# Kernel tuning notes

Measured on AMD Instinct MI355X. Metric: run time of the kernel, lower is better.

Reference implementation:

```python
import jax, jax.numpy as jnp
import numpy as np

N = 100000   # nodes
E = 1600000  # directed edges
F_IN = 100
H = 256
N_LABELS = 19
BN_EPS = 1e-5


def setup_inputs() -> dict:
    key = jax.random.key(0)
    ks = jax.random.split(key, 12)
    p = lambda k, shape, s=0.05: jax.random.normal(k, shape, dtype=jnp.float32) * s
    return {
        "x": jax.random.normal(ks[0], (N, F_IN), dtype=jnp.float32),
        "edge_index": jax.random.randint(ks[1], (2, E), 0, N, dtype=jnp.int32),
        "W1": p(ks[2], (F_IN, F_IN)), "b1": jnp.zeros((F_IN,), jnp.float32),
        "W2": p(ks[3], (F_IN, F_IN)), "b2": jnp.zeros((F_IN,), jnp.float32),
        "W3": p(ks[4], (F_IN, H)),   "b3": jnp.zeros((H,), jnp.float32),
        "fc1_W": p(ks[5], (H, H)),   "fc1_b": jnp.zeros((H,), jnp.float32),
        "fc2a_W": p(ks[6], (H, 128)), "fc2a_b": jnp.zeros((128,), jnp.float32),
        "bn_gamma": jnp.ones((128,), jnp.float32), "bn_beta": jnp.zeros((128,), jnp.float32),
        "fc2b_W": p(ks[7], (128, N_LABELS)), "fc2b_b": jnp.zeros((N_LABELS,), jnp.float32),
    }


def _gcn_conv(x, W, b, src, dst, dinv):
    """PyG GCNConv with add_self_loops + symmetric normalization.
    out[dst] += dinv[src]*dinv[dst] * (x @ W)[src], plus self-loop term, plus bias.
    """
    n = x.shape[0]
    xw = x @ W  # [N, out]
    norm = dinv[src] * dinv[dst]  # [E]
    agg = jax.ops.segment_sum(xw[src] * norm[:, None], dst, num_segments=n)
    agg = agg + xw * (dinv * dinv)[:, None]  # self loops (i -> i)
    return agg + b


def reference(x, edge_index, W1, b1, W2, b2, W3, b3, fc1_W, fc1_b,
              fc2a_W, fc2a_b, bn_gamma, bn_beta, fc2b_W, fc2b_b):
    src, dst = edge_index[0], edge_index[1]
    n = x.shape[0]
    # degree of augmented graph (A + I), computed on targets (sum aggregation)
    deg = jax.ops.segment_sum(jnp.ones((src.shape[0],), x.dtype), dst, num_segments=n) + 1.0
    dinv = jax.lax.rsqrt(deg)

    h = jnp.clip(x, -0.4, 0.4)
    h = jax.nn.relu(_gcn_conv(h, W1, b1, src, dst, dinv))
    h = jax.nn.relu(_gcn_conv(h, W2, b2, src, dst, dinv))
    h = jax.nn.relu(_gcn_conv(h, W3, b3, src, dst, dinv))
    h = jax.nn.relu(h @ fc1_W + fc1_b)
    # fc2: Linear -> BatchNorm1d (train mode, batch stats) -> ReLU -> Linear
    h = h @ fc2a_W + fc2a_b
    mu = jnp.mean(h, axis=0)
    var = jnp.mean(jnp.square(h - mu), axis=0)  # biased var, as torch BN uses
    h = (h - mu) * jax.lax.rsqrt(var + BN_EPS) * bn_gamma + bn_beta
    h = jax.nn.relu(h)
    logits = h @ fc2b_W + fc2b_b
    return jax.nn.log_softmax(logits, axis=1)
```

## Files before the change

### kernel.cpp

```cpp
#include <hip/hip_runtime.h>
#include <hip/hip_bf16.h>

#define N_NODES 100000
#define N_EDGES 1600000
#define F_IN_DIM 100
#define F_IN_PAD 104
#define H_DIM 256
#define BN_DIM 128
#define N_LABELS 19
#define BN_EPS 1e-5f

#define BUCKET_SHIFT 8
#define NB 391
#define EPB 4096
#define PB 391

typedef __attribute__((ext_vector_type(8))) short bf16x8;
typedef __attribute__((ext_vector_type(4))) short s16x4;
typedef __attribute__((ext_vector_type(4))) float f32x4;

static __device__ inline short f2bf(float f) {
    __hip_bfloat16 h = __float2bfloat16(f);
    return *(short*)&h;
}
static __device__ inline float bf2f(short s) {
    unsigned u = ((unsigned)(unsigned short)s) << 16;
    return __builtin_bit_cast(float, u);
}

__global__ __launch_bounds__(256) void part_hist_kernel(const int* __restrict__ dst,
                                                        int* __restrict__ part_hist, int E)
{
    __shared__ int h[NB];
    int tid = threadIdx.x;
    for (int i = tid; i < NB; i += 256) h[i] = 0;
    __syncthreads();
    int base = blockIdx.x * EPB;
    int end = min(base + EPB, E);
    for (int e = base + tid; e < end; e += 256)
        atomicAdd(&h[dst[e] >> BUCKET_SHIFT], 1);
    __syncthreads();
    for (int i = tid; i < NB; i += 256) part_hist[blockIdx.x * NB + i] = h[i];
}

__global__ __launch_bounds__(512) void bucket_total_kernel(const int* __restrict__ part_hist,
                                                           int* __restrict__ bucket_total)
{
    __shared__ int ls[512];
    int b = blockIdx.x;
    int s = 0;
    for (int p = threadIdx.x; p < PB; p += 512) s += part_hist[p * NB + b];
    ls[threadIdx.x] = s;
    __syncthreads();
    for (int off = 256; off > 0; off >>= 1) {
        if (threadIdx.x < off) ls[threadIdx.x] += ls[threadIdx.x + off];
        __syncthreads();
    }
    if (threadIdx.x == 0) bucket_total[b] = ls[0];
}

__global__ __launch_bounds__(512) void bucket_scan_kernel(const int* __restrict__ bucket_total,
                                                          int* __restrict__ bucket_base)
{
    __shared__ int ls[512];
    int tid = threadIdx.x;
    ls[tid] = (tid < NB) ? bucket_total[tid] : 0;
    __syncthreads();
    for (int off = 1; off < 512; off <<= 1) {
        int v = ls[tid];
        int add = (tid >= off) ? ls[tid - off] : 0;
        __syncthreads();
        ls[tid] = v + add;
        __syncthreads();
    }
    if (tid < NB) bucket_base[tid] = (tid > 0) ? ls[tid - 1] : 0;
    if (tid == 0) bucket_base[NB] = ls[NB - 1];
}

__global__ __launch_bounds__(512) void part_offset_kernel(int* __restrict__ part_hist,
                                                          const int* __restrict__ bucket_base)
{
    __shared__ int ls[512];
    int b = blockIdx.x;
    int tid = threadIdx.x;
    int v = (tid < PB) ? part_hist[tid * NB + b] : 0;
    ls[tid] = v;
    __syncthreads();
    for (int off = 1; off < 512; off <<= 1) {
        int x = ls[tid];
        int add = (tid >= off) ? ls[tid - off] : 0;
        __syncthreads();
        ls[tid] = x + add;
        __syncthreads();
    }
    if (tid < PB) part_hist[tid * NB + b] = bucket_base[b] + ((tid > 0) ? ls[tid - 1] : 0);
}

__global__ __launch_bounds__(256) void partition_kernel(const int* __restrict__ src,
                                                        const int* __restrict__ dst,
                                                        const int* __restrict__ part_hist,
                                                        int* __restrict__ ep, int E)
{
    __shared__ int cur[NB];
    int tid = threadIdx.x;
    for (int i = tid; i < NB; i += 256) cur[i] = part_hist[blockIdx.x * NB + i];
    __syncthreads();
    int base = blockIdx.x * EPB;
    int end = min(base + EPB, E);
    for (int e = base + tid; e < end; e += 256) {
        int d = dst[e];
        int s = src[e];
        int pos = atomicAdd(&cur[d >> BUCKET_SHIFT], 1);
        ep[pos] = (s << 8) | (d & 255);
    }
}

__global__ __launch_bounds__(256) void bucket_csr_kernel(const int* __restrict__ ep,
                                                         const int* __restrict__ bucket_base,
                                                         int* __restrict__ row_start,
                                                         float* __restrict__ dinv,
                                                         int* __restrict__ src_sorted, int N, int E)
{
    __shared__ int h[256], sc[256], cur[256];
    int b = blockIdx.x;
    int tid = threadIdx.x;
    int e0 = bucket_base[b], e1 = bucket_base[b + 1];
    int node0 = b << BUCKET_SHIFT;
    int nn = min(256, N - node0);

    h[tid] = 0;
    __syncthreads();
    for (int e = e0 + tid; e < e1; e += 256)
        atomicAdd(&h[ep[e] & 255], 1);
    __syncthreads();

    sc[tid] = h[tid];
    __syncthreads();
    for (int off = 1; off < 256; off <<= 1) {
        int v = sc[tid];
        int add = (tid >= off) ? sc[tid - off] : 0;
        __syncthreads();
        sc[tid] = v + add;
        __syncthreads();
    }
    int excl = e0 + ((tid > 0) ? sc[tid - 1] : 0);
    if (tid < nn) {
        row_start[node0 + tid] = excl;
        dinv[node0 + tid] = rsqrtf((float)h[tid] + 1.0f);
    }
    cur[tid] = excl;
    __syncthreads();
    for (int e = e0 + tid; e < e1; e += 256) {
        int p = ep[e];
        int pos = atomicAdd(&cur[p & 255], 1);
        src_sorted[pos] = ((unsigned)p) >> 8;
    }
    if (b == 0 && tid == 0) row_start[N] = E;
}

__global__ __launch_bounds__(256) void pack_all(
    const float* __restrict__ W1, const float* __restrict__ W2, const float* __restrict__ W3,
    const float* __restrict__ Wf1, const float* __restrict__ Wf2a,
    short* __restrict__ Wt1, short* __restrict__ Wt2, short* __restrict__ Wt3,
    short* __restrict__ Wtf1, short* __restrict__ Wtf2a)
{
    int idx = blockIdx.x * 256 + threadIdx.x;
    const float* W; short* Wt; int K, N, Kp, local;
    if (idx < 10400)       { W = W1;   Wt = Wt1;   K = 100; N = 100; Kp = 104; local = idx; }
    else if (idx < 20800)  { W = W2;   Wt = Wt2;   K = 100; N = 100; Kp = 104; local = idx - 10400; }
    else if (idx < 47424)  { W = W3;   Wt = Wt3;   K = 100; N = 256; Kp = 104; local = idx - 20800; }
    else if (idx < 112960) { W = Wf1;  Wt = Wtf1;  K = 256; N = 256; Kp = 256; local = idx - 47424; }
    else if (idx < 145728) { W = Wf2a; Wt = Wtf2a; K = 256; N = 128; Kp = 256; local = idx - 112960; }
    else return;
    int n = local / Kp, k = local - n * Kp;
    Wt[local] = (k < K) ? f2bf(W[(size_t)k * N + n]) : (short)0;
}

#define SAP 72
template<int ABF16, int OBF16>
__global__ __launch_bounds__(256) void gemm_mfma(
    const void* __restrict__ Av, const short* __restrict__ Wt,
    const float* __restrict__ bias, const float* __restrict__ rowscale,
    void* __restrict__ Cv, int M, int K, int Kp, int Nout,
    int strideA, int strideC, int relu, int doclip)
{
    __shared__ __align__(16) short As[128][SAP];
    __shared__ __align__(16) short Bs[128][SAP];

    int tid = threadIdx.x;
    int wid = tid >> 6;
    int lane = tid & 63;
    int quad = lane >> 4;
    int l15 = lane & 15;
    int wave_m = (wid & 1) * 64;
    int wave_n = (wid >> 1) * 64;
    int rowBase = blockIdx.y * 128;
    int colBase = blockIdx.x * 128;

    f32x4 acc[4][4];
    #pragma unroll
    for (int i = 0; i < 4; i++)
        #pragma unroll
        for (int j = 0; j < 4; j++)
            acc[i][j] = (f32x4){0.f, 0.f, 0.f, 0.f};

    bf16x8 pa[4];
    float4 fa[8];
    bf16x8 pb[4];

    const short* Ab = (const short*)Av;
    const float* Af = (const float*)Av;

    int nIter = (Kp + 63) >> 6;

    auto loadA = [&](int k0) {
        if (ABF16) {
            #pragma unroll
            for (int i = 0; i < 4; i++) {
                int ch = tid + i * 256;
                int r = ch >> 3, c8 = (ch & 7) << 3;
                int gr = rowBase + r, gk = k0 + c8;
                bf16x8 o = (bf16x8){0,0,0,0,0,0,0,0};
                if (gr < M && gk < strideA)
                    o = *(const bf16x8*)(Ab + (size_t)gr * strideA + gk);
                pa[i] = o;
            }
        } else {
            #pragma unroll
            for (int i = 0; i < 8; i++) {
                int ch = tid + i * 256;
                int r = ch >> 4, c4 = (ch & 15) << 2;
                int gr = rowBase + r, gk = k0 + c4;
                float4 v = make_float4(0.f, 0.f, 0.f, 0.f);
                if (gr < M && gk < K)
                    v = *(const float4*)(Af + (size_t)gr * strideA + gk);
                fa[i] = v;
            }
        }
    };
    auto loadB = [&](int k0) {
        #pragma unroll
        for (int i = 0; i < 4; i++) {
            int ch = tid + i * 256;
            int n = ch >> 3, c8 = (ch & 7) << 3;
            int gn = colBase + n, gk = k0 + c8;
            bf16x8 o = (bf16x8){0,0,0,0,0,0,0,0};
            if (gn < Nout && gk < Kp)
                o = *(const bf16x8*)(Wt + (size_t)gn * Kp + gk);
            pb[i] = o;
        }
    };
    auto storeAB = [&]() {
        if (ABF16) {
            #pragma unroll
            for (int i = 0; i < 4; i++) {
                int ch = tid + i * 256;
                int r = ch >> 3, c8 = (ch & 7) << 3;
                *(bf16x8*)(&As[r][c8]) = pa[i];
            }
        } else {
            #pragma unroll
            for (int i = 0; i < 8; i++) {
                int ch = tid + i * 256;
                int r = ch >> 4, c4 = (ch & 15) << 2;
                float4 v = fa[i];
                if (doclip) {
                    v.x = fminf(fmaxf(v.x, -0.4f), 0.4f);
                    v.y = fminf(fmaxf(v.y, -0.4f), 0.4f);
                    v.z = fminf(fmaxf(v.z, -0.4f), 0.4f);
                    v.w = fminf(fmaxf(v.w, -0.4f), 0.4f);
                }
                s16x4 o = (s16x4){f2bf(v.x), f2bf(v.y), f2bf(v.z), f2bf(v.w)};
                *(s16x4*)(&As[r][c4]) = o;
            }
        }
        #pragma unroll
        for (int i = 0; i < 4; i++) {
            int ch = tid + i * 256;
            int n = ch >> 3, c8 = (ch & 7) << 3;
            *(bf16x8*)(&Bs[n][c8]) = pb[i];
        }
    };

    loadA(0); loadB(0);
    for (int it = 0; it < nIter; ++it) {
        if (it > 0) __syncthreads();
        storeAB();
        __syncthreads();
        if (it + 1 < nIter) { loadA((it + 1) << 6); loadB((it + 1) << 6); }
        #pragma unroll
        for (int ks = 0; ks < 2; ks++) {
            bf16x8 a[4], b[4];
            #pragma unroll
            for (int im = 0; im < 4; im++)
                a[im] = *(const bf16x8*)(&As[wave_m + im * 16 + l15][quad * 8 + ks * 32]);
            #pragma unroll
            for (int in = 0; in < 4; in++)
                b[in] = *(const bf16x8*)(&Bs[wave_n + in * 16 + l15][quad * 8 + ks * 32]);
            #pragma unroll
            for (int im = 0; im < 4; im++)
                #pragma unroll
                for (int in = 0; in < 4; in++)
                    acc[im][in] = __builtin_amdgcn_mfma_f32_16x16x32_bf16(
                        a[im], b[in], acc[im][in], 0, 0, 0);
        }
    }

    #pragma unroll
    for (int im = 0; im < 4; im++) {
        #pragma unroll
        for (int reg = 0; reg < 4; reg++) {
            int row = rowBase + wave_m + im * 16 + quad * 4 + reg;
            if (row >= M) continue;
            float rs = rowscale ? rowscale[row] : 1.f;
            #pragma unroll
            for (int in = 0; in < 4; in++) {
                int col = colBase + wave_n + in * 16 + l15;
                float v = 0.f;
                if (col < Nout) {
                    v = acc[im][in][reg];
                    if (bias) v += bias[col];
                    v *= rs;
                    if (relu) v = fmaxf(v, 0.f);
                }
                if (OBF16) {
                    if (col < strideC)
                        ((short*)Cv)[(size_t)row * strideC + col] = f2bf(v);
                } else {
                    if (col < Nout)
                        ((float*)Cv)[(size_t)row * strideC + col] = v;
                }
            }
        }
    }
}

template<int F, int STRIDE, int T, int MODE>
__global__ void gather_kernel(const short* __restrict__ xws,
                              const int* __restrict__ row_start,
                              const int* __restrict__ src_sorted,
                              const float* __restrict__ dinv,
                              const float* __restrict__ bias,
                              short* __restrict__ out, int n)
{
    constexpr int CHUNKS = STRIDE / 8;
    int group = (blockIdx.x * blockDim.x + threadIdx.x) / T;
    int lane = threadIdx.x % T;
    if (group >= n) return;
    int d = group;
    int e0 = row_start[d], e1 = row_start[d + 1];
    bool active = (lane < CHUNKS);
    int coff = lane * 8;
    float acc[8] = {};
    for (int e = e0; e < e1; e++) {
        int s = src_sorted[e];
        if (active) {
            bf16x8 v = *(const bf16x8*)(xws + (size_t)s * STRIDE + coff);
            #pragma unroll
            for (int j = 0; j < 8; j++) acc[j] += bf2f(v[j]);
        }
    }
    if (active) {
        bf16x8 xv = *(const bf16x8*)(xws + (size_t)d * STRIDE + coff);
        float di = dinv[d];
        bf16x8 o;
        #pragma unroll
        for (int j = 0; j < 8; j++) {
            int col = coff + j;
            float v = 0.f;
            if (col < F) {
                v = di * (acc[j] + bf2f(xv[j]));
                if (MODE == 0) v = fmaxf(v + bias[col], 0.f);
                if (MODE == 1) v = di * fmaxf(v + bias[col], 0.f);
            }
            o[j] = f2bf(v);
        }
        *(bf16x8*)(out + (size_t)d * STRIDE + coff) = o;
    }
}

__global__ void bn_stats_kernel(const short* __restrict__ h,
                                float* __restrict__ sum, float* __restrict__ sumsq, int Ntot)
{
    int c = threadIdx.x & 127;
    int rpb = blockDim.x >> 7;
    int r0 = blockIdx.x * rpb + (threadIdx.x >> 7);
    int stride = gridDim.x * rpb;
    float s = 0.f, ss = 0.f;
    for (int r = r0; r < Ntot; r += stride) {
        float v = bf2f(h[(size_t)r * BN_DIM + c]);
        s += v; ss += v * v;
    }
    __shared__ float ls[256], lss[256];
    ls[threadIdx.x] = s; lss[threadIdx.x] = ss;
    __syncthreads();
    if (threadIdx.x < 128) {
        s = ls[threadIdx.x] + ls[threadIdx.x + 128];
        ss = lss[threadIdx.x] + lss[threadIdx.x + 128];
        atomicAdd(&sum[c], s);
        atomicAdd(&sumsq[c], ss);
    }
}

__global__ void bn_finalize_kernel(const float* __restrict__ sum, const float* __restrict__ sumsq,
                                   const float* __restrict__ gamma, const float* __restrict__ beta,
                                   float* __restrict__ a, float* __restrict__ b, int Ntot)
{
    int c = threadIdx.x;
    float inv_n = 1.0f / (float)Ntot;
    float mu = sum[c] * inv_n;
    float var = sumsq[c] * inv_n - mu * mu;
    float ai = gamma[c] * rsqrtf(var + BN_EPS);
    a[c] = ai;
    b[c] = beta[c] - mu * ai;
}

__global__ __launch_bounds__(256) void fc2b_fused_kernel(
    const short* __restrict__ h, const float* __restrict__ bn_a, const float* __restrict__ bn_b,
    const float* __restrict__ W, const float* __restrict__ bias,
    float* __restrict__ out, int Ntot)
{
    __shared__ float Ws[BN_DIM][N_LABELS + 1];
    __shared__ float as[BN_DIM], bs[BN_DIM];
    for (int i = threadIdx.x; i < BN_DIM * N_LABELS; i += 256) {
        int k = i / N_LABELS, j = i - k * N_LABELS;
        Ws[k][j] = W[i];
    }
    if (threadIdx.x < BN_DIM) {
        as[threadIdx.x] = bn_a[threadIdx.x];
        bs[threadIdx.x] = bn_b[threadIdx.x];
    }
    __syncthreads();

    int r = blockIdx.x * 256 + threadIdx.x;
    if (r >= Ntot) return;

    float acc[N_LABELS];
    #pragma unroll
    for (int j = 0; j < N_LABELS; j++) acc[j] = bias[j];

    const short* hr = h + (size_t)r * BN_DIM;
    #pragma unroll
    for (int k0 = 0; k0 < BN_DIM; k0 += 8) {
        bf16x8 hv = *(const bf16x8*)(hr + k0);
        #pragma unroll
        for (int t = 0; t < 8; t++) {
            float v = fmaxf(bf2f(hv[t]) * as[k0 + t] + bs[k0 + t], 0.f);
            #pragma unroll
            for (int j = 0; j < N_LABELS; j++)
                acc[j] = fmaf(v, Ws[k0 + t][j], acc[j]);
        }
    }

    float m = acc[0];
    #pragma unroll
    for (int j = 1; j < N_LABELS; j++) m = fmaxf(m, acc[j]);
    float s = 0.f;
    #pragma unroll
    for (int j = 0; j < N_LABELS; j++) s += expf(acc[j] - m);
    float lse = m + logf(s);
    float* o = out + (size_t)r * N_LABELS;
    #pragma unroll
    for (int j = 0; j < N_LABELS; j++) o[j] = acc[j] - lse;
}

extern "C" void kernel_launch(void* const* d_in, const int* in_sizes, int n_in,
                              void* d_out, int out_size, void* d_ws, size_t ws_size,
                              hipStream_t stream)
{
    const float* x      = (const float*)d_in[0];
    const int*   ei     = (const int*)d_in[1];
    const float* W1     = (const float*)d_in[2];
    const float* b1     = (const float*)d_in[3];
    const float* W2     = (const float*)d_in[4];
    const float* b2     = (const float*)d_in[5];
    const float* W3     = (const float*)d_in[6];
    const float* b3     = (const float*)d_in[7];
    const float* fc1_W  = (const float*)d_in[8];
    const float* fc1_b  = (const float*)d_in[9];
    const float* fc2aW  = (const float*)d_in[10];
    const float* fc2ab  = (const float*)d_in[11];
    const float* gamma  = (const float*)d_in[12];
    const float* beta   = (const float*)d_in[13];
    const float* fc2bW  = (const float*)d_in[14];
    const float* fc2bb  = (const float*)d_in[15];
    float* out = (float*)d_out;

    const int* src = ei;
    const int* dst = ei + N_EDGES;

    char* w = (char*)d_ws;
    float* dinv        = (float*)w;  w += ((size_t)N_NODES * 4 + 255) / 256 * 256;
    int*   row_start   = (int*)w;    w += ((size_t)(N_NODES + 1) * 4 + 255) / 256 * 256;
    int*   part_hist   = (int*)w;    w += ((size_t)PB * NB * 4 + 255) / 256 * 256;
    int*   bucket_total= (int*)w;    w += ((size_t)NB * 4 + 255) / 256 * 256;
    int*   bucket_base = (int*)w;    w += ((size_t)(NB + 1) * 4 + 255) / 256 * 256;
    float* bn_sum      = (float*)w;  w += 128 * 4;
    float* bn_sumsq    = (float*)w;  w += 128 * 4;
    float* bn_a        = (float*)w;  w += 128 * 4;
    float* bn_b        = (float*)w;  w += 128 * 4;
    short* Wt1         = (short*)w;  w += ((size_t)F_IN_DIM * F_IN_PAD * 2 + 255) / 256 * 256;
    short* Wt2         = (short*)w;  w += ((size_t)F_IN_DIM * F_IN_PAD * 2 + 255) / 256 * 256;
    short* Wt3         = (short*)w;  w += ((size_t)H_DIM * F_IN_PAD * 2 + 255) / 256 * 256;
    short* Wtf1        = (short*)w;  w += ((size_t)H_DIM * H_DIM * 2 + 255) / 256 * 256;
    short* Wtf2a       = (short*)w;  w += ((size_t)BN_DIM * H_DIM * 2 + 255) / 256 * 256;
    int*   src_sorted  = (int*)w;    w += ((size_t)N_EDGES * 4 + 255) / 256 * 256;
    int*   ep          = (int*)w;    w += ((size_t)N_EDGES * 4 + 255) / 256 * 256;
    short* xws100      = (short*)w;  w += ((size_t)N_NODES * F_IN_PAD * 2 + 255) / 256 * 256;
    short* agg100      = (short*)w;  w += ((size_t)N_NODES * F_IN_PAD * 2 + 255) / 256 * 256;
    short* big1        = (short*)w;  w += ((size_t)N_NODES * H_DIM * 2 + 255) / 256 * 256;
    short* big2        = (short*)w;  w += ((size_t)N_NODES * H_DIM * 2 + 255) / 256 * 256;

    part_hist_kernel<<<PB, 256, 0, stream>>>(dst, part_hist, N_EDGES);
    bucket_total_kernel<<<NB, 512, 0, stream>>>(part_hist, bucket_total);
    bucket_scan_kernel<<<1, 512, 0, stream>>>(bucket_total, bucket_base);
    part_offset_kernel<<<NB, 512, 0, stream>>>(part_hist, bucket_base);
    partition_kernel<<<PB, 256, 0, stream>>>(src, dst, part_hist, ep, N_EDGES);
    bucket_csr_kernel<<<NB, 256, 0, stream>>>(ep, bucket_base, row_start, dinv,
                                              src_sorted, N_NODES, N_EDGES);

    pack_all<<<570, 256, 0, stream>>>(W1, W2, W3, fc1_W, fc2aW, Wt1, Wt2, Wt3, Wtf1, Wtf2a);

    dim3 g100(1, (N_NODES + 127) / 128);
    dim3 g256(2, (N_NODES + 127) / 128);
    int gatherBlocks = (N_NODES * 16 + 255) / 256;

    gemm_mfma<0, 1><<<g100, 256, 0, stream>>>(x, Wt1, nullptr, dinv, xws100,
        N_NODES, F_IN_DIM, F_IN_PAD, F_IN_DIM, F_IN_DIM, F_IN_PAD, 0, 1);
    gather_kernel<F_IN_DIM, F_IN_PAD, 16, 0><<<gatherBlocks, 256, 0, stream>>>(
        xws100, row_start, src_sorted, dinv, b1, agg100, N_NODES);

    gemm_mfma<1, 1><<<g100, 256, 0, stream>>>(agg100, Wt2, nullptr, dinv, xws100,
        N_NODES, F_IN_DIM, F_IN_PAD, F_IN_DIM, F_IN_PAD, F_IN_PAD, 0, 0);
    gather_kernel<F_IN_DIM, F_IN_PAD, 16, 1><<<gatherBlocks, 256, 0, stream>>>(
        xws100, row_start, src_sorted, dinv, b2, agg100, N_NODES);

    gather_kernel<F_IN_DIM, F_IN_PAD, 16, 2><<<gatherBlocks, 256, 0, stream>>>(
        agg100, row_start, src_sorted, dinv, nullptr, xws100, N_NODES);
    gemm_mfma<1, 1><<<g256, 256, 0, stream>>>(xws100, Wt3, b3, nullptr, big1,
        N_NODES, F_IN_DIM, F_IN_PAD, H_DIM, F_IN_PAD, H_DIM, 1, 0);

    gemm_mfma<1, 1><<<g256, 256, 0, stream>>>(big1, Wtf1, fc1_b, nullptr, big2,
        N_NODES, H_DIM, H_DIM, H_DIM, H_DIM, H_DIM, 1, 0);

    gemm_mfma<1, 1><<<g100, 256, 0, stream>>>(big2, Wtf2a, fc2ab, nullptr, big1,
        N_NODES, H_DIM, H_DIM, BN_DIM, H_DIM, BN_DIM, 0, 0);

    hipMemsetAsync(bn_sum, 0, 2 * 128 * 4, stream);
    bn_stats_kernel<<<512, 256, 0, stream>>>(big1, bn_sum, bn_sumsq, N_NODES);
    bn_finalize_kernel<<<1, 128, 0, stream>>>(bn_sum, bn_sumsq, gamma, beta, bn_a, bn_b, N_NODES);

    fc2b_fused_kernel<<<(N_NODES + 255) / 256, 256, 0, stream>>>(
        big1, bn_a, bn_b, fc2bW, fc2bb, out, N_NODES);
}
```

Measured before the change: 735.6 us.

## Replace tiled GEMM with persistent weight-stationary streaming MFMA kernel

Replaces the 128x128 double-tiled GEMM with a persistent kernel. Each block loads its full weight slice into XOR-swizzled LDS once. Each wave then streams 16-row A tiles straight from global memory into MFMA with no A staging in LDS and no per-K-step barriers. The fp32 clip-and-cast of x moves into a separate pre-pass kernel that writes padded bf16, so every GEMM takes bf16 input. This aims to remove repeated weight reloads and syncs in these skinny-K GEMMs, at the cost of an extra pass over x and less A reuse across output columns.

```diff
diff --git a/kernel.cpp b/kernel.cpp
--- a/kernel.cpp
+++ b/kernel.cpp
@@ -16,7 +16,6 @@
 #define PB 391
 
 typedef __attribute__((ext_vector_type(8))) short bf16x8;
-typedef __attribute__((ext_vector_type(4))) short s16x4;
 typedef __attribute__((ext_vector_type(4))) float f32x4;
 
 static __device__ inline short f2bf(float f) {
@@ -176,160 +175,103 @@
     Wt[local] = (k < K) ? f2bf(W[(size_t)k * N + n]) : (short)0;
 }
 
-#define SAP 72
-template<int ABF16, int OBF16>
-__global__ __launch_bounds__(256) void gemm_mfma(
-    const void* __restrict__ Av, const short* __restrict__ Wt,
+__global__ __launch_bounds__(256) void clip_cast_kernel(const float* __restrict__ x,
+                                                        short* __restrict__ xbf)
+{
+    int idx = blockIdx.x * 256 + threadIdx.x;
+    if (idx >= N_NODES * 13) return;
+    int r = idx / 13, c8 = (idx - r * 13) * 8;
+    const float* xr = x + (size_t)r * F_IN_DIM;
+    bf16x8 o;
+    #pragma unroll
+    for (int j = 0; j < 8; j++) {
+        int c = c8 + j;
+        float v = (c < F_IN_DIM) ? xr[c] : 0.f;
+        v = fminf(fmaxf(v, -0.4f), 0.4f);
+        o[j] = f2bf(v);
+    }
+    *(bf16x8*)(xbf + (size_t)r * F_IN_PAD + c8) = o;
+}
+
+template<int KP_MEM, int KP_STG, int NOUT_TILE>
+__global__ __launch_bounds__(512) void gemm_stream(
+    const short* __restrict__ A, const short* __restrict__ Wt,
     const float* __restrict__ bias, const float* __restrict__ rowscale,
-    void* __restrict__ Cv, int M, int K, int Kp, int Nout,
-    int strideA, int strideC, int relu, int doclip)
-{
-    __shared__ __align__(16) short As[128][SAP];
-    __shared__ __align__(16) short Bs[128][SAP];
-
-    int tid = threadIdx.x;
-    int wid = tid >> 6;
+    short* __restrict__ C, int M, int Nout, int strideA, int strideC, int relu)
+{
+    constexpr int NC = NOUT_TILE / 16;
+    constexpr int KC = KP_STG / 32;
+    constexpr int CPR = KP_STG / 8;
+    __shared__ __align__(16) short Bs[NOUT_TILE * KP_STG];
+
+    int tid = threadIdx.x;
+    int colBase = blockIdx.y * NOUT_TILE;
+
+    for (int ch = tid; ch < NOUT_TILE * CPR; ch += 512) {
+        int n = ch / CPR, c = ch - n * CPR;
+        int c8 = c * 8;
+        bf16x8 o = (bf16x8){0,0,0,0,0,0,0,0};
+        int gn = colBase + n;
+        if (gn < Nout && c8 + 8 <= KP_MEM)
+            o = *(const bf16x8*)(Wt + (size_t)gn * KP_MEM + c8);
+        *(bf16x8*)(&Bs[n * KP_STG + ((c ^ (n & 7)) << 3)]) = o;
+    }
+    __syncthreads();
+
+    int wv = tid >> 6;
     int lane = tid & 63;
-    int quad = lane >> 4;
-    int l15 = lane & 15;
-    int wave_m = (wid & 1) * 64;
-    int wave_n = (wid >> 1) * 64;
-    int rowBase = blockIdx.y * 128;
-    int colBase = blockIdx.x * 128;
-
-    f32x4 acc[4][4];
-    #pragma unroll
-    for (int i = 0; i < 4; i++)
-        #pragma unroll
-        for (int j = 0; j < 4; j++)
-            acc[i][j] = (f32x4){0.f, 0.f, 0.f, 0.f};
-
-    bf16x8 pa[4];
-    float4 fa[8];
-    bf16x8 pb[4];
-
-    const short* Ab = (const short*)Av;
-    const float* Af = (const float*)Av;
-
-    int nIter = (Kp + 63) >> 6;
-
-    auto loadA = [&](int k0) {
-        if (ABF16) {
+    int quad = lane >> 4, l15 = lane & 15;
+    int nTiles = (M + 15) >> 4;
+    int gw = blockIdx.x * 8 + wv;
+    int stride = gridDim.x * 8;
+
+    for (int t = gw; t < nTiles; t += stride) {
+        int m0 = t << 4;
+        int row = m0 + l15;
+        bool rok = row < M;
+        const short* Ar = A + (size_t)row * strideA;
+
+        f32x4 acc[NC];
+        #pragma unroll
+        for (int nc = 0; nc < NC; nc++) acc[nc] = (f32x4){0.f, 0.f, 0.f, 0.f};
+
+        #pragma unroll
+        for (int kc = 0; kc < KC; kc++) {
+            int off = kc * 32 + quad * 8;
+            bf16x8 a = (bf16x8){0,0,0,0,0,0,0,0};
+            if (rok && off < KP_MEM)
+                a = *(const bf16x8*)(Ar + off);
+            int c = kc * 4 + quad;
             #pragma unroll
-            for (int i = 0; i < 4; i++) {
-                int ch = tid + i * 256;
-                int r = ch >> 3, c8 = (ch & 7) << 3;
-                int gr = rowBase + r, gk = k0 + c8;
-                bf16x8 o = (bf16x8){0,0,0,0,0,0,0,0};
-                if (gr < M && gk < strideA)
-                    o = *(const bf16x8*)(Ab + (size_t)gr * strideA + gk);
-                pa[i] = o;
+            for (int nc = 0; nc < NC; nc++) {
+                int n = nc * 16 + l15;
+                bf16x8 b = *(const bf16x8*)(&Bs[n * KP_STG + ((c ^ (n & 7)) << 3)]);
+                acc[nc] = __builtin_amdgcn_mfma_f32_16x16x32_bf16(a, b, acc[nc], 0, 0, 0);
             }
-        } else {
+        }
+
+        float rs[4];
+        #pragma unroll
+        for (int reg = 0; reg < 4; reg++) {
+            int r = m0 + quad * 4 + reg;
+            rs[reg] = (rowscale && r < M) ? rowscale[r] : 1.f;
+        }
+        #pragma unroll
+        for (int nc = 0; nc < NC; nc++) {
+            int col = colBase + nc * 16 + l15;
+            if (col >= strideC) continue;
+            bool cvalid = col < Nout;
+            float bv = (bias && cvalid) ? bias[col] : 0.f;
             #pragma unroll
-            for (int i = 0; i < 8; i++) {
-                int ch = tid + i * 256;
-                int r = ch >> 4, c4 = (ch & 15) << 2;
-                int gr = rowBase + r, gk = k0 + c4;
-                float4 v = make_float4(0.f, 0.f, 0.f, 0.f);
-                if (gr < M && gk < K)
-                    v = *(const float4*)(Af + (size_t)gr * strideA + gk);
-                fa[i] = v;
-            }
-        }
-    };
-    auto loadB = [&](int k0) {
-        #pragma unroll
-        for (int i = 0; i < 4; i++) {
-            int ch = tid + i * 256;
-            int n = ch >> 3, c8 = (ch & 7) << 3;
-            int gn = colBase + n, gk = k0 + c8;
-            bf16x8 o = (bf16x8){0,0,0,0,0,0,0,0};
-            if (gn < Nout && gk < Kp)
-                o = *(const bf16x8*)(Wt + (size_t)gn * Kp + gk);
-            pb[i] = o;
-        }
-    };
-    auto storeAB = [&]() {
-        if (ABF16) {
-            #pragma unroll
-            for (int i = 0; i < 4; i++) {
-                int ch = tid + i * 256;
-                int r = ch >> 3, c8 = (ch & 7) << 3;
-                *(bf16x8*)(&As[r][c8]) = pa[i];
-            }
-        } else {
-            #pragma unroll
-            for (int i = 0; i < 8; i++) {
-                int ch = tid + i * 256;
-                int r = ch >> 4, c4 = (ch & 15) << 2;
-                float4 v = fa[i];
-                if (doclip) {
-                    v.x = fminf(fmaxf(v.x, -0.4f), 0.4f);
-                    v.y = fminf(fmaxf(v.y, -0.4f), 0.4f);
-                    v.z = fminf(fmaxf(v.z, -0.4f), 0.4f);
-                    v.w = fminf(fmaxf(v.w, -0.4f), 0.4f);
-                }
-                s16x4 o = (s16x4){f2bf(v.x), f2bf(v.y), f2bf(v.z), f2bf(v.w)};
-                *(s16x4*)(&As[r][c4]) = o;
-            }
-        }
-        #pragma unroll
-        for (int i = 0; i < 4; i++) {
-            int ch = tid + i * 256;
-            int n = ch >> 3, c8 = (ch & 7) << 3;
-            *(bf16x8*)(&Bs[n][c8]) = pb[i];
-        }
-    };
-
-    loadA(0); loadB(0);
-    for (int it = 0; it < nIter; ++it) {
-        if (it > 0) __syncthreads();
-        storeAB();
-        __syncthreads();
-        if (it + 1 < nIter) { loadA((it + 1) << 6); loadB((it + 1) << 6); }
-        #pragma unroll
-        for (int ks = 0; ks < 2; ks++) {
-            bf16x8 a[4], b[4];
-            #pragma unroll
-            for (int im = 0; im < 4; im++)
-                a[im] = *(const bf16x8*)(&As[wave_m + im * 16 + l15][quad * 8 + ks * 32]);
-            #pragma unroll
-            for (int in = 0; in < 4; in++)
-                b[in] = *(const bf16x8*)(&Bs[wave_n + in * 16 + l15][quad * 8 + ks * 32]);
-            #pragma unroll
-            for (int im = 0; im < 4; im++)
-                #pragma unroll
-                for (int in = 0; in < 4; in++)
-                    acc[im][in] = __builtin_amdgcn_mfma_f32_16x16x32_bf16(
-                        a[im], b[in], acc[im][in], 0, 0, 0);
-        }
-    }
-
-    #pragma unroll
-    for (int im = 0; im < 4; im++) {
-        #pragma unroll
-        for (int reg = 0; reg < 4; reg++) {
-            int row = rowBase + wave_m + im * 16 + quad * 4 + reg;
-            if (row >= M) continue;
-            float rs = rowscale ? rowscale[row] : 1.f;
-            #pragma unroll
-            for (int in = 0; in < 4; in++) {
-                int col = colBase + wave_n + in * 16 + l15;
+            for (int reg = 0; reg < 4; reg++) {
+                int r = m0 + quad * 4 + reg;
+                if (r >= M) continue;
                 float v = 0.f;
-                if (col < Nout) {
-                    v = acc[im][in][reg];
-                    if (bias) v += bias[col];
-                    v *= rs;
+                if (cvalid) {
+                    v = (acc[nc][reg] + bv) * rs[reg];
                     if (relu) v = fmaxf(v, 0.f);
                 }
-                if (OBF16) {
-                    if (col < strideC)
-                        ((short*)Cv)[(size_t)row * strideC + col] = f2bf(v);
-                } else {
-                    if (col < Nout)
-                        ((float*)Cv)[(size_t)row * strideC + col] = v;
-                }
+                C[(size_t)r * strideC + col] = f2bf(v);
             }
         }
     }
@@ -506,6 +448,7 @@
     short* Wtf2a       = (short*)w;  w += ((size_t)BN_DIM * H_DIM * 2 + 255) / 256 * 256;
     int*   src_sorted  = (int*)w;    w += ((size_t)N_EDGES * 4 + 255) / 256 * 256;
     int*   ep          = (int*)w;    w += ((size_t)N_EDGES * 4 + 255) / 256 * 256;
+    short* xbf         = (short*)w;  w += ((size_t)N_NODES * F_IN_PAD * 2 + 255) / 256 * 256;
     short* xws100      = (short*)w;  w += ((size_t)N_NODES * F_IN_PAD * 2 + 255) / 256 * 256;
     short* agg100      = (short*)w;  w += ((size_t)N_NODES * F_IN_PAD * 2 + 255) / 256 * 256;
     short* big1        = (short*)w;  w += ((size_t)N_NODES * H_DIM * 2 + 255) / 256 * 256;
@@ -520,31 +463,30 @@
                                               src_sorted, N_NODES, N_EDGES);
 
     pack_all<<<570, 256, 0, stream>>>(W1, W2, W3, fc1_W, fc2aW, Wt1, Wt2, Wt3, Wtf1, Wtf2a);
-
-    dim3 g100(1, (N_NODES + 127) / 128);
-    dim3 g256(2, (N_NODES + 127) / 128);
+    clip_cast_kernel<<<(N_NODES * 13 + 255) / 256, 256, 0, stream>>>(x, xbf);
+
     int gatherBlocks = (N_NODES * 16 + 255) / 256;
 
-    gemm_mfma<0, 1><<<g100, 256, 0, stream>>>(x, Wt1, nullptr, dinv, xws100,
-        N_NODES, F_IN_DIM, F_IN_PAD, F_IN_DIM, F_IN_DIM, F_IN_PAD, 0, 1);
+    gemm_stream<104, 128, 112><<<dim3(512, 1), 512, 0, stream>>>(
+        xbf, Wt1, nullptr, dinv, xws100, N_NODES, F_IN_DIM, F_IN_PAD, F_IN_PAD, 0);
     gather_kernel<F_IN_DIM, F_IN_PAD, 16, 0><<<gatherBlocks, 256, 0, stream>>>(
         xws100, row_start, src_sorted, dinv, b1, agg100, N_NODES);
 
-    gemm_mfma<1, 1><<<g100, 256, 0, stream>>>(agg100, Wt2, nullptr, dinv, xws100,
-        N_NODES, F_IN_DIM, F_IN_PAD, F_IN_DIM, F_IN_PAD, F_IN_PAD, 0, 0);
+    gemm_stream<104, 128, 112><<<dim3(512, 1), 512, 0, stream>>>(
+        agg100, Wt2, nullptr, dinv, xws100, N_NODES, F_IN_DIM, F_IN_PAD, F_IN_PAD, 0);
     gather_kernel<F_IN_DIM, F_IN_PAD, 16, 1><<<gatherBlocks, 256, 0, stream>>>(
         xws100, row_start, src_sorted, dinv, b2, agg100, N_NODES);
 
     gather_kernel<F_IN_DIM, F_IN_PAD, 16, 2><<<gatherBlocks, 256, 0, stream>>>(
         agg100, row_start, src_sorted, dinv, nullptr, xws100, N_NODES);
-    gemm_mfma<1, 1><<<g256, 256, 0, stream>>>(xws100, Wt3, b3, nullptr, big1,
-        N_NODES, F_IN_DIM, F_IN_PAD, H_DIM, F_IN_PAD, H_DIM, 1, 0);
-
-    gemm_mfma<1, 1><<<g256, 256, 0, stream>>>(big1, Wtf1, fc1_b, nullptr, big2,
-        N_NODES, H_DIM, H_DIM, H_DIM, H_DIM, H_DIM, 1, 0);
-
-    gemm_mfma<1, 1><<<g100, 256, 0, stream>>>(big2, Wtf2a, fc2ab, nullptr, big1,
-        N_NODES, H_DIM, H_DIM, BN_DIM, H_DIM, BN_DIM, 0, 0);
+    gemm_stream<104, 128, 128><<<dim3(384, 2), 512, 0, stream>>>(
+        xws100, Wt3, b3, nullptr, big1, N_NODES, H_DIM, F_IN_PAD, H_DIM, 1);
+
+    gemm_stream<256, 256, 128><<<dim3(256, 2), 512, 0, stream>>>(
+        big1, Wtf1, fc1_b, nullptr, big2, N_NODES, H_DIM, H_DIM, H_DIM, 1);
+
+    gemm_stream<256, 256, 128><<<dim3(512, 1), 512, 0, stream>>>(
+        big2, Wtf2a, fc2ab, nullptr, big1, N_NODES, BN_DIM, H_DIM, BN_DIM, 0);
 
     hipMemsetAsync(bn_sum, 0, 2 * 128 * 4, stream);
     bn_stats_kernel<<<512, 256, 0, stream>>>(big1, bn_sum, bn_sumsq, N_NODES);
```

Result: slower. 820.1 us (+11.5%).
